# Kernel optimization log

Hardware: AMD Instinct MI355X
Metric: run time of the kernel (lower is better)

The kernel has to match this reference:

```python
import jax, jax.numpy as jnp
import numpy as np

N = 30000      # nodes
E = 480000     # edges (before self-loops)
IN = 128       # in_dim
HID = 256      # hidden_dim
HEADS = 4
C = HID // HEADS  # per-head channels = 64
NEG_SLOPE = 0.2


def setup_inputs() -> dict:
    key = jax.random.key(0)
    ks = jax.random.split(key, 12)
    s_in = 1.0 / np.sqrt(IN)
    s_h = 1.0 / np.sqrt(HID)
    return {
        "x": jax.random.normal(ks[0], (N, IN), dtype=jnp.float32),
        "edge_index": jax.random.randint(ks[1], (2, E), 0, N, dtype=jnp.int32),
        # GAT layer 1 (in: IN -> HEADS*C)
        "W1": jax.random.normal(ks[2], (IN, HID), dtype=jnp.float32) * s_in,
        "att_src1": jax.random.normal(ks[3], (HEADS, C), dtype=jnp.float32) * s_h,
        "att_dst1": jax.random.normal(ks[4], (HEADS, C), dtype=jnp.float32) * s_h,
        "b1": jnp.zeros((HID,), dtype=jnp.float32),
        # GAT layer 2 (in: HID -> HEADS*C)
        "W2": jax.random.normal(ks[5], (HID, HID), dtype=jnp.float32) * s_h,
        "att_src2": jax.random.normal(ks[6], (HEADS, C), dtype=jnp.float32) * s_h,
        "att_dst2": jax.random.normal(ks[7], (HEADS, C), dtype=jnp.float32) * s_h,
        "b2": jnp.zeros((HID,), dtype=jnp.float32),
        # LayerNorms
        "g1": jnp.ones((HID,), dtype=jnp.float32),
        "be1": jnp.zeros((HID,), dtype=jnp.float32),
        "g2": jnp.ones((HID,), dtype=jnp.float32),
        "be2": jnp.zeros((HID,), dtype=jnp.float32),
        # residual projection (in_dim != hidden_dim)
        "Wp": jax.random.normal(ks[8], (IN, HID), dtype=jnp.float32) * s_in,
        "bp": jnp.zeros((HID,), dtype=jnp.float32),
    }


def layer_norm(x, g, b, eps=1e-5):
    mu = jnp.mean(x, axis=-1, keepdims=True)
    var = jnp.var(x, axis=-1, keepdims=True)
    return (x - mu) * jax.lax.rsqrt(var + eps) * g + b


def gat_conv(x, src, dst, W, a_src, a_dst, bias):
    """PyG-style GATConv (concat heads). src/dst already include self-loops."""
    n = x.shape[0]
    h = (x @ W).reshape(n, HEADS, C)                     # (N, H, C)
    e_src = jnp.sum(h * a_src, axis=-1)                  # (N, H)
    e_dst = jnp.sum(h * a_dst, axis=-1)                  # (N, H)
    e = jax.nn.leaky_relu(e_src[src] + e_dst[dst], NEG_SLOPE)  # (Etot, H)
    # per-destination segment softmax (numerically stable)
    e_max = jax.lax.stop_gradient(jax.ops.segment_max(e, dst, num_segments=n))
    p = jnp.exp(e - e_max[dst])
    denom = jax.ops.segment_sum(p, dst, num_segments=n)[dst]
    alpha = p / denom                                    # (Etot, H)
    out = jax.ops.segment_sum(h[src] * alpha[..., None], dst, num_segments=n)
    return out.reshape(n, HID) + bias


def reference(x, edge_index, W1, att_src1, att_dst1, b1, W2, att_src2, att_dst2, b2,
              g1, be1, g2, be2, Wp, bp):
    n = x.shape[0]
    loop = jnp.arange(n, dtype=edge_index.dtype)
    src = jnp.concatenate([edge_index[0], loop])
    dst = jnp.concatenate([edge_index[1], loop])

    residual = x @ Wp + bp                               # proj residual
    h = gat_conv(x, src, dst, W1, att_src1, att_dst1, b1)
    h = jax.nn.elu(layer_norm(h + residual, g1, be1))
    # dropout is identity at inference
    residual = h
    h2 = gat_conv(h, src, dst, W2, att_src2, att_dst2, b2)
    out = jax.nn.elu(layer_norm(h2 + residual, g2, be2))
    return out
```

## Files before the change

kernel.cpp:

```cpp
#include <hip/hip_runtime.h>
#include <cstdint>
#include <cstddef>

#define N_NODES 30000
#define E_EDGES 480000
#define ETOT    510000
#define IN_DIM  128
#define HID     256
#define HEADS   4
#define NEG_SLOPE 0.2f
#define DEG_BLOCKS 1993

static inline int cdiv(int a, int b){ return (a + b - 1) / b; }

typedef short bf16x8 __attribute__((ext_vector_type(8)));
typedef float f32x4  __attribute__((ext_vector_type(4)));
typedef float f32x2  __attribute__((ext_vector_type(2)));

__device__ __forceinline__ unsigned short f2bf(float f) {
  unsigned u = __float_as_uint(f);
  unsigned r = (u + 0x7FFFu + ((u >> 16) & 1u)) >> 16;
  return (unsigned short)r;
}
__device__ __forceinline__ float bf2f(unsigned short s) {
  return __uint_as_float((unsigned)s << 16);
}
__device__ __forceinline__ unsigned char f2fp8(float v) {
  return (unsigned char)(__builtin_amdgcn_cvt_pk_fp8_f32(v, v, 0, false) & 0xFF);
}

__global__ __launch_bounds__(256) void setup(
    const int* __restrict__ ei, int* __restrict__ deg,
    const float* __restrict__ x, const float* __restrict__ W1,
    const float* __restrict__ Wp, const float* __restrict__ W2,
    ushort* __restrict__ xbf, ushort* __restrict__ w1t,
    ushort* __restrict__ wpt, ushort* __restrict__ w2t)
{
  int b = blockIdx.x;
  int t = threadIdx.x;
  if (b < DEG_BLOCKS) {
    int e = b * 256 + t;
    if (e < ETOT) {
      int d = (e < E_EDGES) ? ei[E_EDGES + e] : (e - E_EDGES);
      atomicAdd(&deg[d], 1);
    }
    return;
  }
  b -= DEG_BLOCKS;
  if (b < 3750) {
    int i = b * 256 + t;
    float4 v = ((const float4*)x)[i];
    ushort4 o;
    o.x = f2bf(v.x); o.y = f2bf(v.y); o.z = f2bf(v.z); o.w = f2bf(v.w);
    ((ushort4*)xbf)[i] = o;
  } else if (b < 3750 + 128) {
    int k = b - 3750;
    w1t[(size_t)t * IN_DIM + k] = f2bf(W1[(size_t)k * HID + t]);
  } else if (b < 3750 + 256) {
    int k = b - 3878;
    wpt[(size_t)t * IN_DIM + k] = f2bf(Wp[(size_t)k * HID + t]);
  } else {
    int k = b - 4006;
    w2t[(size_t)t * HID + k] = f2bf(W2[(size_t)k * HID + t]);
  }
}

template<int K, bool L1>
__global__ __launch_bounds__(256) void gemm_fused(
    const ushort* __restrict__ A,
    const ushort* __restrict__ WT,
    const float* __restrict__ att_src, const float* __restrict__ att_dst,
    unsigned char* __restrict__ hout, float* __restrict__ esrc, float* __restrict__ edst,
    ushort* __restrict__ rout, const float* __restrict__ pbias, int n)
{
  const int wave = threadIdx.x >> 6;
  const int lane = threadIdx.x & 63;
  const int wr = wave >> 1, wc = wave & 1;
  const int brow = blockIdx.x * 128 + wr * 64;
  const int bcol = blockIdx.y * 128 + wc * 64;
  const int lrow = lane & 15;
  const int kgrp = lane >> 4;

  f32x4 acc[4][4] = {};
  for (int k0 = 0; k0 < K; k0 += 32) {
    const int kb = k0 + kgrp * 8;
    bf16x8 a[4], b[4];
    #pragma unroll
    for (int mi = 0; mi < 4; ++mi) {
      int r = brow + mi * 16 + lrow;
      r = min(r, n - 1);
      a[mi] = *(const bf16x8*)&A[(size_t)r * K + kb];
    }
    #pragma unroll
    for (int ni = 0; ni < 4; ++ni) {
      int c = bcol + ni * 16 + lrow;
      b[ni] = *(const bf16x8*)&WT[(size_t)c * K + kb];
    }
    #pragma unroll
    for (int mi = 0; mi < 4; ++mi)
      #pragma unroll
      for (int ni = 0; ni < 4; ++ni)
        acc[mi][ni] = __builtin_amdgcn_mfma_f32_16x16x32_bf16(a[mi], b[ni], acc[mi][ni], 0, 0, 0);
  }
  const bool proj = L1 && (bcol >= 256);
  #pragma unroll
  for (int mi = 0; mi < 4; ++mi) {
    #pragma unroll
    for (int r = 0; r < 4; ++r) {
      int row = brow + mi * 16 + kgrp * 4 + r;
      if (row < n) {
        #pragma unroll
        for (int ni = 0; ni < 4; ++ni) {
          int colg = bcol + ni * 16 + lrow;
          float v = acc[mi][ni][r];
          if (proj) {
            int c = colg - 256;
            rout[(size_t)row * HID + c] = f2bf(v + pbias[c]);
          } else {
            hout[(size_t)row * HID + colg] = f2fp8(v);
          }
        }
      }
    }
  }
  if (!proj) {
    const int hh = bcol >> 6;
    float as[4], ad[4];
    #pragma unroll
    for (int ni = 0; ni < 4; ++ni) {
      as[ni] = att_src[hh * 64 + ni * 16 + lrow];
      ad[ni] = att_dst[hh * 64 + ni * 16 + lrow];
    }
    #pragma unroll
    for (int mi = 0; mi < 4; ++mi) {
      #pragma unroll
      for (int r = 0; r < 4; ++r) {
        float vs = 0.f, vd = 0.f;
        #pragma unroll
        for (int ni = 0; ni < 4; ++ni) {
          float c = acc[mi][ni][r];
          vs += c * as[ni];
          vd += c * ad[ni];
        }
        #pragma unroll
        for (int m = 1; m <= 8; m <<= 1) {
          vs += __shfl_xor(vs, m);
          vd += __shfl_xor(vd, m);
        }
        int row = brow + mi * 16 + kgrp * 4 + r;
        if (lrow == 0 && row < n) {
          esrc[row * HEADS + hh] = vs;
          edst[row * HEADS + hh] = vd;
        }
      }
    }
  }
}

__global__ __launch_bounds__(1024) void scan_rowptr(const int* __restrict__ deg,
                                                    int* __restrict__ rowptr,
                                                    int* __restrict__ cursor)
{
  const int CE = 30;
  __shared__ int sc[1024];
  int t = threadIdx.x;
  int base = t * CE;
  int local[CE];
  int s = 0;
  #pragma unroll
  for (int i = 0; i < CE; ++i) {
    int idx = base + i;
    int v = (idx < N_NODES) ? deg[idx] : 0;
    local[i] = s;
    s += v;
  }
  sc[t] = s;
  __syncthreads();
  for (int o = 1; o < 1024; o <<= 1) {
    int v = (t >= o) ? sc[t - o] : 0;
    __syncthreads();
    sc[t] += v;
    __syncthreads();
  }
  int off = sc[t] - s;
  #pragma unroll
  for (int i = 0; i < CE; ++i) {
    int idx = base + i;
    if (idx < N_NODES) {
      rowptr[idx] = off + local[i];
      cursor[idx] = off + local[i];
    }
  }
  if (t == 1023) rowptr[N_NODES] = off + s;
}

__global__ __launch_bounds__(256) void scatter_edges(const int* __restrict__ ei,
                                                     int* __restrict__ cursor,
                                                     int* __restrict__ col)
{
  int e = blockIdx.x * blockDim.x + threadIdx.x;
  if (e >= ETOT) return;
  int s, d;
  if (e < E_EDGES) { s = ei[e]; d = ei[E_EDGES + e]; }
  else             { s = d = e - E_EDGES; }
  int pos = atomicAdd(&cursor[d], 1);
  col[pos] = s;
}

template<bool WRITE_BF16>
__global__ __launch_bounds__(256) void gat_agg(
    const int* __restrict__ rowptr, const int* __restrict__ col,
    const float* __restrict__ esrc, const float* __restrict__ edst,
    const unsigned char* __restrict__ h8, const float* __restrict__ bias,
    const ushort* __restrict__ resid, const float* __restrict__ gamma,
    const float* __restrict__ beta, float* __restrict__ out_f32,
    ushort* __restrict__ out_bf16)
{
  const int wave = threadIdx.x >> 6;
  const int lane = threadIdx.x & 63;
  const int d = blockIdx.x * 4 + wave;
  const int slot = lane >> 4;
  const int cblk = (lane & 15) * 16;
  const int headc = (lane & 15) >> 2;
  const int r0 = rowptr[d], r1 = rowptr[d + 1];

  const float edh = edst[d * HEADS + headc];
  f32x2 acc2[8] = {};
  float dp = 0.f;

  for (int j = r0 + slot; j < r1; j += 4) {
    int s = col[j];
    float v = esrc[s * HEADS + headc] + edh;
    v = (v >= 0.f) ? v : NEG_SLOPE * v;
    float p = __expf(v);
    dp += p;
    f32x2 p2 = { p, p };
    uint4 w = *(const uint4*)&h8[(size_t)s * HID + cblk];
    unsigned wd[4] = { w.x, w.y, w.z, w.w };
    #pragma unroll
    for (int q = 0; q < 4; ++q) {
      f32x2 lo = __builtin_amdgcn_cvt_pk_f32_fp8(wd[q], false);
      f32x2 hi = __builtin_amdgcn_cvt_pk_f32_fp8(wd[q], true);
      acc2[2 * q]     += lo * p2;
      acc2[2 * q + 1] += hi * p2;
    }
  }

  #pragma unroll
  for (int q = 0; q < 8; ++q) {
    #pragma unroll
    for (int m = 16; m <= 32; m <<= 1) {
      acc2[q].x += __shfl_xor(acc2[q].x, m);
      acc2[q].y += __shfl_xor(acc2[q].y, m);
    }
  }
  dp += __shfl_xor(dp, 16);
  dp += __shfl_xor(dp, 32);
  float rden = 1.f / dp;

  f32x2 v2[8];
  {
    const uint4* rp = (const uint4*)&resid[(size_t)d * HID + cblk];
    uint4 r0v = rp[0], r1v = rp[1];
    unsigned rd[8] = { r0v.x, r0v.y, r0v.z, r0v.w, r1v.x, r1v.y, r1v.z, r1v.w };
    const f32x2* b2 = (const f32x2*)&bias[cblk];
    f32x2 rden2 = { rden, rden };
    #pragma unroll
    for (int q = 0; q < 8; ++q) {
      f32x2 rw;
      rw.x = __uint_as_float(rd[q] << 16);
      rw.y = __uint_as_float(rd[q] & 0xffff0000u);
      v2[q] = acc2[q] * rden2 + b2[q] + rw;
    }
  }

  float s1 = 0.f, s2 = 0.f;
  #pragma unroll
  for (int q = 0; q < 8; ++q) {
    s1 += v2[q].x + v2[q].y;
    s2 += v2[q].x * v2[q].x + v2[q].y * v2[q].y;
  }
  #pragma unroll
  for (int m = 1; m <= 32; m <<= 1) {
    s1 += __shfl_xor(s1, m);
    s2 += __shfl_xor(s2, m);
  }
  float mu = s1 * (1.f / 1024.f);
  float var = s2 * (1.f / 1024.f) - mu * mu;
  float rr = rsqrtf(var + 1e-5f);

  if (slot == 0) {
    const f32x2* g2 = (const f32x2*)&gamma[cblk];
    const f32x2* e2 = (const f32x2*)&beta[cblk];
    float y[16];
    #pragma unroll
    for (int q = 0; q < 8; ++q) {
      f32x2 g = g2[q], e = e2[q];
      float t0 = (v2[q].x - mu) * rr * g.x + e.x;
      float t1 = (v2[q].y - mu) * rr * g.y + e.y;
      y[2 * q]     = (t0 > 0.f) ? t0 : expm1f(t0);
      y[2 * q + 1] = (t1 > 0.f) ? t1 : expm1f(t1);
    }
    if (WRITE_BF16) {
      uint4 o[2];
      #pragma unroll
      for (int q = 0; q < 8; ++q) {
        unsigned wv = (unsigned)f2bf(y[2 * q]) | ((unsigned)f2bf(y[2 * q + 1]) << 16);
        ((unsigned*)o)[q] = wv;
      }
      uint4* op = (uint4*)&out_bf16[(size_t)d * HID + cblk];
      op[0] = o[0]; op[1] = o[1];
    } else {
      float4* op = (float4*)&out_f32[(size_t)d * HID + cblk];
      #pragma unroll
      for (int q = 0; q < 4; ++q) {
        float4 ov = { y[4 * q], y[4 * q + 1], y[4 * q + 2], y[4 * q + 3] };
        op[q] = ov;
      }
    }
  }
}

extern "C" void kernel_launch(void* const* d_in, const int* in_sizes, int n_in,
                              void* d_out, int out_size, void* d_ws, size_t ws_size,
                              hipStream_t stream) {
  const float* x   = (const float*)d_in[0];
  const int*   ei  = (const int*)d_in[1];
  const float* W1  = (const float*)d_in[2];
  const float* as1 = (const float*)d_in[3];
  const float* ad1 = (const float*)d_in[4];
  const float* b1  = (const float*)d_in[5];
  const float* W2  = (const float*)d_in[6];
  const float* as2 = (const float*)d_in[7];
  const float* ad2 = (const float*)d_in[8];
  const float* b2  = (const float*)d_in[9];
  const float* g1  = (const float*)d_in[10];
  const float* be1 = (const float*)d_in[11];
  const float* g2  = (const float*)d_in[12];
  const float* be2 = (const float*)d_in[13];
  const float* Wp  = (const float*)d_in[14];
  const float* bp  = (const float*)d_in[15];
  float* out = (float*)d_out;

  const size_t NB16 = (size_t)N_NODES * HID * sizeof(ushort);
  const size_t NB8  = (size_t)N_NODES * HID;
  const size_t XB16 = (size_t)N_NODES * IN_DIM * sizeof(ushort);
  const size_t NH_BUF = (size_t)N_NODES * HEADS * sizeof(float);
  char* ws = (char*)d_ws;
  size_t off = 0;
  unsigned char* h8 = (unsigned char*)(ws + off); off += NB8;
  ushort* hAbf  = (ushort*)(ws + off); off += NB16;
  ushort* rbf   = (ushort*)(ws + off); off += NB16;
  ushort* xbf   = (ushort*)(ws + off); off += XB16;
  ushort* w1t   = (ushort*)(ws + off); off += (size_t)HID * IN_DIM * 2;
  ushort* wpt   = (ushort*)(ws + off); off += (size_t)HID * IN_DIM * 2;
  ushort* w2t   = (ushort*)(ws + off); off += (size_t)HID * HID * 2;
  float*  esrc  = (float*) (ws + off); off += NH_BUF;
  float*  edstb = (float*) (ws + off); off += NH_BUF;
  int*    deg    = (int*)(ws + off); off += (size_t)N_NODES * 4;
  int*    rowptr = (int*)(ws + off); off += (size_t)(N_NODES + 1) * 4;
  int*    cursor = (int*)(ws + off); off += (size_t)N_NODES * 4;
  int*    col    = (int*)(ws + off); off += (size_t)ETOT * 4;

  hipMemsetAsync(deg, 0, (size_t)N_NODES * 4, stream);
  setup<<<DEG_BLOCKS + 3750 + 128 + 128 + 256, 256, 0, stream>>>(
      ei, deg, x, W1, Wp, W2, xbf, w1t, wpt, w2t);
  scan_rowptr<<<1, 1024, 0, stream>>>(deg, rowptr, cursor);
  scatter_edges<<<cdiv(ETOT, 256), 256, 0, stream>>>(ei, cursor, col);

  gemm_fused<IN_DIM, true><<<dim3(cdiv(N_NODES, 128), 4), 256, 0, stream>>>(
      xbf, w1t, as1, ad1, h8, esrc, edstb, rbf, bp, N_NODES);
  gat_agg<true><<<N_NODES / 4, 256, 0, stream>>>(
      rowptr, col, esrc, edstb, h8, b1, rbf, g1, be1, nullptr, hAbf);

  gemm_fused<HID, false><<<dim3(cdiv(N_NODES, 128), 2), 256, 0, stream>>>(
      hAbf, w2t, as2, ad2, h8, esrc, edstb, nullptr, nullptr, N_NODES);
  gat_agg<false><<<N_NODES / 4, 256, 0, stream>>>(
      rowptr, col, esrc, edstb, h8, b2, hAbf, g2, be2, out, nullptr);
}
```

Measured before the change: 247.0 us.

## Map one destination node per 16 lanes and batch 8 neighbor gathers per iteration

The aggregation kernel now gives each destination node 16 lanes instead of a full 64-lane wave split into 4 edge slots. This removes the cross-slot shuffle reduction and the idle-lane epilogue. Each thread walks all of its node's edges and loads 8 neighbor indices, scores and fp8 feature rows at once to expose more memory-level parallelism. The costs are more registers per thread and longer serial loops for high-degree nodes, with clamped loads and zeroed weights for the tail edges.

```diff
diff --git a/kernel.cpp b/kernel.cpp
--- a/kernel.cpp
+++ b/kernel.cpp
@@ -216,46 +216,47 @@
     const float* __restrict__ beta, float* __restrict__ out_f32,
     ushort* __restrict__ out_bf16)
 {
-  const int wave = threadIdx.x >> 6;
-  const int lane = threadIdx.x & 63;
-  const int d = blockIdx.x * 4 + wave;
-  const int slot = lane >> 4;
-  const int cblk = (lane & 15) * 16;
-  const int headc = (lane & 15) >> 2;
+  const int t = threadIdx.x;
+  const int lane16 = t & 15;
+  const int d = blockIdx.x * 16 + (t >> 4);
+  const int cblk = lane16 * 16;
+  const int headc = lane16 >> 2;
   const int r0 = rowptr[d], r1 = rowptr[d + 1];
 
   const float edh = edst[d * HEADS + headc];
   f32x2 acc2[8] = {};
   float dp = 0.f;
 
-  for (int j = r0 + slot; j < r1; j += 4) {
-    int s = col[j];
-    float v = esrc[s * HEADS + headc] + edh;
-    v = (v >= 0.f) ? v : NEG_SLOPE * v;
-    float p = __expf(v);
-    dp += p;
-    f32x2 p2 = { p, p };
-    uint4 w = *(const uint4*)&h8[(size_t)s * HID + cblk];
-    unsigned wd[4] = { w.x, w.y, w.z, w.w };
-    #pragma unroll
-    for (int q = 0; q < 4; ++q) {
-      f32x2 lo = __builtin_amdgcn_cvt_pk_f32_fp8(wd[q], false);
-      f32x2 hi = __builtin_amdgcn_cvt_pk_f32_fp8(wd[q], true);
-      acc2[2 * q]     += lo * p2;
-      acc2[2 * q + 1] += hi * p2;
-    }
-  }
-
-  #pragma unroll
-  for (int q = 0; q < 8; ++q) {
-    #pragma unroll
-    for (int m = 16; m <= 32; m <<= 1) {
-      acc2[q].x += __shfl_xor(acc2[q].x, m);
-      acc2[q].y += __shfl_xor(acc2[q].y, m);
-    }
-  }
-  dp += __shfl_xor(dp, 16);
-  dp += __shfl_xor(dp, 32);
+  for (int j = r0; j < r1; j += 8) {
+    int s[8];
+    #pragma unroll
+    for (int i = 0; i < 8; ++i) s[i] = col[min(j + i, r1 - 1)];
+    float es[8];
+    #pragma unroll
+    for (int i = 0; i < 8; ++i) es[i] = esrc[s[i] * HEADS + headc];
+    uint4 w[8];
+    #pragma unroll
+    for (int i = 0; i < 8; ++i)
+      w[i] = *(const uint4*)&h8[(size_t)s[i] * HID + cblk];
+    #pragma unroll
+    for (int i = 0; i < 8; ++i) {
+      float v = es[i] + edh;
+      v = (v >= 0.f) ? v : NEG_SLOPE * v;
+      float p = (j + i < r1) ? __expf(v) : 0.f;
+      dp += p;
+      f32x2 p2 = { p, p };
+      unsigned wd0 = w[i].x, wd1 = w[i].y, wd2 = w[i].z, wd3 = w[i].w;
+      acc2[0] += __builtin_amdgcn_cvt_pk_f32_fp8(wd0, false) * p2;
+      acc2[1] += __builtin_amdgcn_cvt_pk_f32_fp8(wd0, true)  * p2;
+      acc2[2] += __builtin_amdgcn_cvt_pk_f32_fp8(wd1, false) * p2;
+      acc2[3] += __builtin_amdgcn_cvt_pk_f32_fp8(wd1, true)  * p2;
+      acc2[4] += __builtin_amdgcn_cvt_pk_f32_fp8(wd2, false) * p2;
+      acc2[5] += __builtin_amdgcn_cvt_pk_f32_fp8(wd2, true)  * p2;
+      acc2[6] += __builtin_amdgcn_cvt_pk_f32_fp8(wd3, false) * p2;
+      acc2[7] += __builtin_amdgcn_cvt_pk_f32_fp8(wd3, true)  * p2;
+    }
+  }
+
   float rden = 1.f / dp;
 
   f32x2 v2[8];
@@ -281,42 +282,40 @@
     s2 += v2[q].x * v2[q].x + v2[q].y * v2[q].y;
   }
   #pragma unroll
-  for (int m = 1; m <= 32; m <<= 1) {
+  for (int m = 1; m <= 8; m <<= 1) {
     s1 += __shfl_xor(s1, m);
     s2 += __shfl_xor(s2, m);
   }
-  float mu = s1 * (1.f / 1024.f);
-  float var = s2 * (1.f / 1024.f) - mu * mu;
+  float mu = s1 * (1.f / HID);
+  float var = s2 * (1.f / HID) - mu * mu;
   float rr = rsqrtf(var + 1e-5f);
 
-  if (slot == 0) {
-    const f32x2* g2 = (const f32x2*)&gamma[cblk];
-    const f32x2* e2 = (const f32x2*)&beta[cblk];
-    float y[16];
+  const f32x2* g2 = (const f32x2*)&gamma[cblk];
+  const f32x2* e2 = (const f32x2*)&beta[cblk];
+  float y[16];
+  #pragma unroll
+  for (int q = 0; q < 8; ++q) {
+    f32x2 g = g2[q], e = e2[q];
+    float t0 = (v2[q].x - mu) * rr * g.x + e.x;
+    float t1 = (v2[q].y - mu) * rr * g.y + e.y;
+    y[2 * q]     = (t0 > 0.f) ? t0 : expm1f(t0);
+    y[2 * q + 1] = (t1 > 0.f) ? t1 : expm1f(t1);
+  }
+  if (WRITE_BF16) {
+    uint4 o[2];
     #pragma unroll
     for (int q = 0; q < 8; ++q) {
-      f32x2 g = g2[q], e = e2[q];
-      float t0 = (v2[q].x - mu) * rr * g.x + e.x;
-      float t1 = (v2[q].y - mu) * rr * g.y + e.y;
-      y[2 * q]     = (t0 > 0.f) ? t0 : expm1f(t0);
-      y[2 * q + 1] = (t1 > 0.f) ? t1 : expm1f(t1);
-    }
-    if (WRITE_BF16) {
-      uint4 o[2];
-      #pragma unroll
-      for (int q = 0; q < 8; ++q) {
-        unsigned wv = (unsigned)f2bf(y[2 * q]) | ((unsigned)f2bf(y[2 * q + 1]) << 16);
-        ((unsigned*)o)[q] = wv;
-      }
-      uint4* op = (uint4*)&out_bf16[(size_t)d * HID + cblk];
-      op[0] = o[0]; op[1] = o[1];
-    } else {
-      float4* op = (float4*)&out_f32[(size_t)d * HID + cblk];
-      #pragma unroll
-      for (int q = 0; q < 4; ++q) {
-        float4 ov = { y[4 * q], y[4 * q + 1], y[4 * q + 2], y[4 * q + 3] };
-        op[q] = ov;
-      }
+      unsigned wv = (unsigned)f2bf(y[2 * q]) | ((unsigned)f2bf(y[2 * q + 1]) << 16);
+      ((unsigned*)o)[q] = wv;
+    }
+    uint4* op = (uint4*)&out_bf16[(size_t)d * HID + cblk];
+    op[0] = o[0]; op[1] = o[1];
+  } else {
+    float4* op = (float4*)&out_f32[(size_t)d * HID + cblk];
+    #pragma unroll
+    for (int q = 0; q < 4; ++q) {
+      float4 ov = { y[4 * q], y[4 * q + 1], y[4 * q + 2], y[4 * q + 3] };
+      op[q] = ov;
     }
   }
 }
@@ -370,11 +369,11 @@
 
   gemm_fused<IN_DIM, true><<<dim3(cdiv(N_NODES, 128), 4), 256, 0, stream>>>(
       xbf, w1t, as1, ad1, h8, esrc, edstb, rbf, bp, N_NODES);
-  gat_agg<true><<<N_NODES / 4, 256, 0, stream>>>(
+  gat_agg<true><<<N_NODES / 16, 256, 0, stream>>>(
       rowptr, col, esrc, edstb, h8, b1, rbf, g1, be1, nullptr, hAbf);
 
   gemm_fused<HID, false><<<dim3(cdiv(N_NODES, 128), 2), 256, 0, stream>>>(
       hAbf, w2t, as2, ad2, h8, esrc, edstb, nullptr, nullptr, N_NODES);
-  gat_agg<false><<<N_NODES / 4, 256, 0, stream>>>(
+  gat_agg<false><<<N_NODES / 16, 256, 0, stream>>>(
       rowptr, col, esrc, edstb, h8, b2, hAbf, g2, be2, out, nullptr);
 }
```

Result: faster. 218.1 us (-11.7%).
